# Kernel optimization log

Hardware: AMD Instinct MI355X
Metric: run time of the kernel (lower is better)

## Reference

```python
import jax, jax.numpy as jnp
import numpy as np

SCALING = 32.0 / 16  # alpha / rank


def setup_inputs() -> dict:
    key = jax.random.key(0)
    k1, k2, k3, k4, k5 = jax.random.split(key, 5)
    B, S, D_IN, D_OUT, R = 4, 2048, 4096, 4096, 16
    inputs = jax.random.normal(k1, (B, S, D_IN), dtype=jnp.float32)
    weight = jax.random.normal(k2, (D_OUT, D_IN), dtype=jnp.float32) * (1.0 / np.sqrt(D_IN))
    bias = jax.random.normal(k3, (D_OUT,), dtype=jnp.float32)
    lora_a = jax.random.normal(k4, (R, D_IN), dtype=jnp.float32) * (1.0 / np.sqrt(D_IN))
    lora_b = jax.random.normal(k5, (D_OUT, R), dtype=jnp.float32) * (1.0 / np.sqrt(R))
    return {"inputs": inputs, "weight": weight, "bias": bias, "lora_a": lora_a, "lora_b": lora_b}


def reference(inputs, weight, bias, lora_a, lora_b):
    # base = x @ W^T + b
    base = jnp.einsum("bsd,od->bso", inputs, weight) + bias
    # low-rank update: x @ (B A)^T * s, computed as two skinny matmuls
    # (mathematically identical to torch's full-rank materialization)
    xa = jnp.einsum("bsd,rd->bsr", inputs, lora_a)   # [B,S,R]
    update = jnp.einsum("bsr,or->bso", xa, lora_b)    # [B,S,O]
    return base + update * SCALING
```

## Files before the change

### kernel.cpp

```cpp
#include <hip/hip_runtime.h>
#include <hip/hip_bf16.h>
#include <stdint.h>


typedef __bf16 bf16x8 __attribute__((ext_vector_type(8)));
typedef __bf16 bf16x4 __attribute__((ext_vector_type(4)));
typedef float f32x4 __attribute__((ext_vector_type(4)));

#define LORA_R 16

__device__ __forceinline__ void async_copy16(const void* g, void* l) {
  __builtin_amdgcn_global_load_lds(
      (const __attribute__((address_space(1))) void*)g,
      (__attribute__((address_space(3))) void*)l, 16, 0, 0);
}


__global__ __launch_bounds__(256) void pack_x_kernel(
    const float* __restrict__ X, __hip_bfloat16* __restrict__ Xp, int K) {
  const int lane = threadIdx.x & 63;
  const int wave = threadIdx.x >> 6;
  const int nkb = K >> 5;
  const int kb = blockIdx.x * 4 + wave;
  const int mb = blockIdx.y;
  const int row = (mb << 4) + (lane & 15);
  const int col = (kb << 5) + ((lane >> 4) << 3);
  const float* src = X + (size_t)row * K + col;
  f32x4 v0 = *(const f32x4*)src;
  f32x4 v1 = *(const f32x4*)(src + 4);
  bf16x8 o;
#pragma unroll
  for (int j = 0; j < 4; ++j) { o[j] = (__bf16)v0[j]; o[4 + j] = (__bf16)v1[j]; }
  *(bf16x8*)((char*)Xp + ((size_t)(mb * nkb + kb) << 10) + (lane << 4)) = o;
}

__global__ __launch_bounds__(256) void foldpack_w_kernel(
    const float* __restrict__ W, const float* __restrict__ A,
    const float* __restrict__ Bl, __hip_bfloat16* __restrict__ Wp, int K) {
  const int lane = threadIdx.x & 63;
  const int wave = threadIdx.x >> 6;
  const int nkb = K >> 5;
  const int kb = blockIdx.x * 4 + wave;
  const int nb = blockIdx.y;
  const int n = (nb << 4) + (lane & 15);
  const int col = (kb << 5) + ((lane >> 4) << 3);
  float res[8];
  {
    f32x4 w0 = *(const f32x4*)(W + (size_t)n * K + col);
    f32x4 w1 = *(const f32x4*)(W + (size_t)n * K + col + 4);
#pragma unroll
    for (int j = 0; j < 4; ++j) { res[j] = w0[j]; res[4 + j] = w1[j]; }
  }
#pragma unroll
  for (int r = 0; r < LORA_R; ++r) {
    const float b2 = 2.0f * Bl[n * LORA_R + r];
    f32x4 a0 = *(const f32x4*)(A + (size_t)r * K + col);
    f32x4 a1 = *(const f32x4*)(A + (size_t)r * K + col + 4);
#pragma unroll
    for (int j = 0; j < 4; ++j) { res[j] += b2 * a0[j]; res[4 + j] += b2 * a1[j]; }
  }
  bf16x8 o;
#pragma unroll
  for (int j = 0; j < 8; ++j) o[j] = (__bf16)res[j];
  *(bf16x8*)((char*)Wp + ((size_t)(nb * nkb + kb) << 10) + (lane << 4)) = o;
}

__global__ __launch_bounds__(512, 2) void gemm_pipelined(
    const __hip_bfloat16* __restrict__ Xp,
    const __hip_bfloat16* __restrict__ Wp,
    const float* __restrict__ bias,
    float* __restrict__ Out, int M, int N, int K) {
  __shared__ __align__(16) char lds[131072];

  const int tid = threadIdx.x;
  const int lane = tid & 63;
  const int wave = tid >> 6;
  const int wm = wave >> 2;
  const int wn = wave & 3;

  const int nwg = gridDim.x;
  const int bid = blockIdx.x;
  const int swz = (bid & 7) * (nwg >> 3) + (bid >> 3);
  const int ntn = N >> 8;
  const int tm = swz / ntn;
  const int tn = swz - tm * ntn;

  const int nkb = K >> 5;
  const int nt = nkb;

  const char* aSrc = (const char*)Xp +
      ((size_t)((tm << 4) + wave) * nkb << 10) + (lane << 4);
  const char* bSrc = (const char*)Wp +
      ((size_t)((tn << 4) + wave) * nkb << 10) + (lane << 4);
  const size_t siteStride = (size_t)8 * nkb << 10;

  char* ldsA = lds + (wave << 10);
  char* ldsB = lds + 16384 + (wave << 10);
  const char* ldsRdA = lds + (wm << 13) + (lane << 4);
  const char* ldsRdB = lds + 16384 + (wn << 12) + (lane << 4);

  f32x4 acc[8][4];
#pragma unroll
  for (int i = 0; i < 8; ++i)
#pragma unroll
    for (int j = 0; j < 4; ++j) acc[i][j] = (f32x4){0.f, 0.f, 0.f, 0.f};

#pragma unroll
  for (int pt = 0; pt < 3; ++pt) {
    const int bo = pt << 15;
    async_copy16(aSrc + ((size_t)pt << 10), ldsA + bo);
    async_copy16(aSrc + siteStride + ((size_t)pt << 10), ldsA + bo + 8192);
    async_copy16(bSrc + ((size_t)pt << 10), ldsB + bo);
    async_copy16(bSrc + siteStride + ((size_t)pt << 10), ldsB + bo + 8192);
  }
  asm volatile("s_waitcnt vmcnt(8)" ::: "memory");
  __builtin_amdgcn_s_barrier();

  bf16x8 af[4], bv[4];
  for (int t = 0; t < nt - 3; ++t) {
    const int buf = t & 3;
    const int pb = (t + 3) & 3;
    const size_t kOff = (size_t)(t + 3) << 10;
    const char* aP = ldsRdA + (buf << 15);
    const char* bP = ldsRdB + (buf << 15);
#pragma unroll
    for (int i = 0; i < 4; ++i) af[i] = *(const bf16x8*)(aP + (i << 10));
#pragma unroll
    for (int i = 0; i < 4; ++i) bv[i] = *(const bf16x8*)(bP + (i << 10));
    async_copy16(aSrc + kOff, ldsA + (pb << 15));
    async_copy16(aSrc + siteStride + kOff, ldsA + (pb << 15) + 8192);
    __builtin_amdgcn_s_barrier();
    asm volatile("s_waitcnt lgkmcnt(0)" ::: "memory");
    __builtin_amdgcn_sched_barrier(0);
    __builtin_amdgcn_s_setprio(1);
#pragma unroll
    for (int mi = 0; mi < 4; ++mi)
#pragma unroll
      for (int ni = 0; ni < 4; ++ni)
        acc[mi][ni] = __builtin_amdgcn_mfma_f32_16x16x32_bf16(
            af[mi], bv[ni], acc[mi][ni], 0, 0, 0);
    __builtin_amdgcn_s_setprio(0);
    __builtin_amdgcn_s_barrier();
#pragma unroll
    for (int i = 0; i < 4; ++i) af[i] = *(const bf16x8*)(aP + 4096 + (i << 10));
    async_copy16(bSrc + kOff, ldsB + (pb << 15));
    async_copy16(bSrc + siteStride + kOff, ldsB + (pb << 15) + 8192);
    asm volatile("s_waitcnt vmcnt(8)" ::: "memory");
    __builtin_amdgcn_s_barrier();
    asm volatile("s_waitcnt lgkmcnt(0)" ::: "memory");
    __builtin_amdgcn_sched_barrier(0);
    __builtin_amdgcn_s_setprio(1);
#pragma unroll
    for (int mi = 0; mi < 4; ++mi)
#pragma unroll
      for (int ni = 0; ni < 4; ++ni)
        acc[4 + mi][ni] = __builtin_amdgcn_mfma_f32_16x16x32_bf16(
            af[mi], bv[ni], acc[4 + mi][ni], 0, 0, 0);
    __builtin_amdgcn_s_setprio(0);
    __builtin_amdgcn_s_barrier();
  }
  asm volatile("s_waitcnt vmcnt(0)" ::: "memory");
  __builtin_amdgcn_s_barrier();
  for (int t = nt - 3; t < nt; ++t) {
    const int buf = t & 3;
    const char* aP = ldsRdA + (buf << 15);
    const char* bP = ldsRdB + (buf << 15);
#pragma unroll
    for (int i = 0; i < 4; ++i) af[i] = *(const bf16x8*)(aP + (i << 10));
#pragma unroll
    for (int i = 0; i < 4; ++i) bv[i] = *(const bf16x8*)(bP + (i << 10));
#pragma unroll
    for (int mi = 0; mi < 4; ++mi)
#pragma unroll
      for (int ni = 0; ni < 4; ++ni)
        acc[mi][ni] = __builtin_amdgcn_mfma_f32_16x16x32_bf16(
            af[mi], bv[ni], acc[mi][ni], 0, 0, 0);
#pragma unroll
    for (int i = 0; i < 4; ++i) af[i] = *(const bf16x8*)(aP + 4096 + (i << 10));
#pragma unroll
    for (int mi = 0; mi < 4; ++mi)
#pragma unroll
      for (int ni = 0; ni < 4; ++ni)
        acc[4 + mi][ni] = __builtin_amdgcn_mfma_f32_16x16x32_bf16(
            af[mi], bv[ni], acc[4 + mi][ni], 0, 0, 0);
  }

  const int col = lane & 15;
  const int quad = lane >> 4;
  const int m0 = tm << 8;
  const int n0 = tn << 8;
#pragma unroll
  for (int ni = 0; ni < 4; ++ni) {
    const int n = n0 + wn * 64 + ni * 16 + col;
    const float bvs = bias[n];
#pragma unroll
    for (int mi = 0; mi < 8; ++mi) {
      const size_t rowBase = (size_t)(m0 + wm * 128 + mi * 16 + quad * 4) * N + n;
#pragma unroll
      for (int r = 0; r < 4; ++r)
        Out[rowBase + (size_t)r * N] = acc[mi][ni][r] + bvs;
    }
  }
}

#define BM 128
#define BN 128
#define BK 32

__global__ void foldcast_w_kernel(const float* __restrict__ W,
                                  const float* __restrict__ A,
                                  const float* __restrict__ Bl,
                                  __hip_bfloat16* __restrict__ Wp, int K) {
  const int n = blockIdx.y;
  const int k = blockIdx.x * 256 + threadIdx.x;
  float acc = W[(size_t)n * K + k];
#pragma unroll
  for (int r = 0; r < LORA_R; ++r)
    acc += 2.0f * Bl[n * LORA_R + r] * A[(size_t)r * K + k];
  Wp[(size_t)n * K + k] = __float2bfloat16(acc);
}

__global__ void padb32_kernel(const float* __restrict__ lB,
                              __hip_bfloat16* __restrict__ B32) {
  const int i = blockIdx.x * 256 + threadIdx.x;
  const int n = i >> 5, r = i & 31;
  B32[i] = (r < LORA_R) ? __float2bfloat16(lB[n * LORA_R + r])
                        : __float2bfloat16(0.0f);
}

__global__ __launch_bounds__(256) void xa_fp32_kernel(
    const float* __restrict__ X, const float* __restrict__ A,
    __hip_bfloat16* __restrict__ XA32, int K) {
  const int lane = threadIdx.x & 63;
  const int m = blockIdx.x * 4 + (threadIdx.x >> 6);
  float acc[LORA_R] = {};
  const size_t xrow = (size_t)m * K;
  for (int k0 = 0; k0 < K; k0 += 256) {
    const int k = k0 + lane * 4;
    f32x4 xv = *(const f32x4*)(X + xrow + k);
#pragma unroll
    for (int r = 0; r < LORA_R; ++r) {
      f32x4 av = *(const f32x4*)(A + (size_t)r * K + k);
      acc[r] += xv[0] * av[0] + xv[1] * av[1] + xv[2] * av[2] + xv[3] * av[3];
    }
  }
#pragma unroll
  for (int r = 0; r < LORA_R; ++r)
    for (int off = 32; off > 0; off >>= 1) acc[r] += __shfl_xor(acc[r], off, 64);
  if (lane == 0) {
#pragma unroll
    for (int r = 0; r < LORA_R; ++r)
      XA32[(size_t)m * 32 + r] = __float2bfloat16(acc[r]);
#pragma unroll
    for (int r = LORA_R; r < 32; ++r)
      XA32[(size_t)m * 32 + r] = __float2bfloat16(0.0f);
  }
}

template <bool XPRE, bool WPRE, bool ELORA>
__global__ __launch_bounds__(256) void gemm_kernel(
    const void* __restrict__ Xv, const void* __restrict__ Wv,
    const float* __restrict__ bias,
    const __hip_bfloat16* __restrict__ XA32,
    const __hip_bfloat16* __restrict__ B32,
    float* __restrict__ Out, int M, int N, int K) {
  __shared__ __align__(16) unsigned short As[BM * BK];
  __shared__ __align__(16) unsigned short Bs[BN * BK];

  const int t = threadIdx.x;
  const int lane = t & 63;
  const int wave = t >> 6;
  const int m0 = blockIdx.y * BM;
  const int n0 = blockIdx.x * BN;
  const int wm = (wave >> 1) * 64;
  const int wn = (wave & 1) * 64;

  const int srow = t >> 2;
  const int ka = (t & 3) * 8;
  const int f_r = t >> 3;
  const int f_c = (t & 7) * 4;

  char* smA = (char*)As;
  char* smB = (char*)Bs;
  const int waveByte = wave * 1024;

  f32x4 acc[4][4];
#pragma unroll
  for (int mi = 0; mi < 4; ++mi)
#pragma unroll
    for (int ni = 0; ni < 4; ++ni) acc[mi][ni] = (f32x4){0.f, 0.f, 0.f, 0.f};

  const unsigned short* aBase = As + (wm + (lane & 15)) * BK + (lane >> 4) * 8;
  const unsigned short* bBase = Bs + (wn + (lane & 15)) * BK + (lane >> 4) * 8;

  const int kIters = K / BK;
  for (int kt = 0; kt < kIters; ++kt) {
    const int gk = kt * BK;
    if constexpr (XPRE) {
      const __hip_bfloat16* Xb = (const __hip_bfloat16*)Xv;
      async_copy16(Xb + (size_t)(m0 + srow) * K + gk + ka, smA + waveByte);
      async_copy16(Xb + (size_t)(m0 + 64 + srow) * K + gk + ka, smA + 4096 + waveByte);
    } else {
      const float* Xf = (const float*)Xv;
#pragma unroll
      for (int j = 0; j < 4; ++j) {
        const int row = j * 32 + f_r;
        f32x4 v = *(const f32x4*)(Xf + (size_t)(m0 + row) * K + gk + f_c);
        bf16x4 p;
#pragma unroll
        for (int e = 0; e < 4; ++e) p[e] = (__bf16)v[e];
        *(bf16x4*)(smA + row * 64 + f_c * 2) = p;
      }
    }
    if constexpr (WPRE) {
      const __hip_bfloat16* Wb = (const __hip_bfloat16*)Wv;
      async_copy16(Wb + (size_t)(n0 + srow) * K + gk + ka, smB + waveByte);
      async_copy16(Wb + (size_t)(n0 + 64 + srow) * K + gk + ka, smB + 4096 + waveByte);
    } else {
      const float* Wf = (const float*)Wv;
#pragma unroll
      for (int j = 0; j < 4; ++j) {
        const int row = j * 32 + f_r;
        f32x4 v = *(const f32x4*)(Wf + (size_t)(n0 + row) * K + gk + f_c);
        bf16x4 p;
#pragma unroll
        for (int e = 0; e < 4; ++e) p[e] = (__bf16)v[e];
        *(bf16x4*)(smB + row * 64 + f_c * 2) = p;
      }
    }
    __syncthreads();

    bf16x8 af[4], bfv[4];
#pragma unroll
    for (int i = 0; i < 4; ++i) {
      af[i] = *(const bf16x8*)(aBase + i * 16 * BK);
      bfv[i] = *(const bf16x8*)(bBase + i * 16 * BK);
    }
#pragma unroll
    for (int mi = 0; mi < 4; ++mi)
#pragma unroll
      for (int ni = 0; ni < 4; ++ni)
        acc[mi][ni] = __builtin_amdgcn_mfma_f32_16x16x32_bf16(
            af[mi], bfv[ni], acc[mi][ni], 0, 0, 0);
    __syncthreads();
  }

  const int col = lane & 15;
  const int quad = lane >> 4;
  const int rbase = quad * 4;

  bf16x8 xaf[4], blf[4];
  if constexpr (ELORA) {
#pragma unroll
    for (int mi = 0; mi < 4; ++mi)
      xaf[mi] = *(const bf16x8*)(XA32 + (size_t)(m0 + wm + mi * 16 + col) * 32 + quad * 8);
#pragma unroll
    for (int ni = 0; ni < 4; ++ni)
      blf[ni] = *(const bf16x8*)(B32 + (size_t)(n0 + wn + ni * 16 + col) * 32 + quad * 8);
  }

  const f32x4 zero4 = (f32x4){0.f, 0.f, 0.f, 0.f};
#pragma unroll
  for (int ni = 0; ni < 4; ++ni) {
    const int n = n0 + wn + ni * 16 + col;
    const float bv = bias[n];
#pragma unroll
    for (int mi = 0; mi < 4; ++mi) {
      f32x4 u = zero4;
      if constexpr (ELORA)
        u = __builtin_amdgcn_mfma_f32_16x16x32_bf16(xaf[mi], blf[ni], zero4, 0, 0, 0);
      const size_t rowBase = (size_t)(m0 + wm + mi * 16 + rbase) * N + n;
#pragma unroll
      for (int r = 0; r < 4; ++r)
        Out[rowBase + (size_t)r * N] = acc[mi][ni][r] + bv + 2.0f * u[r];
    }
  }
}

extern "C" void kernel_launch(void* const* d_in, const int* in_sizes, int n_in,
                              void* d_out, int out_size, void* d_ws, size_t ws_size,
                              hipStream_t stream) {
  const float* X    = (const float*)d_in[0];
  const float* W    = (const float*)d_in[1];
  const float* bias = (const float*)d_in[2];
  const float* lA   = (const float*)d_in[3];
  const float* lB   = (const float*)d_in[4];
  float* Out = (float*)d_out;

  const int K = in_sizes[3] / LORA_R;
  const int N = in_sizes[2];
  const int M = in_sizes[0] / K;

  const size_t xbBytes = (size_t)M * K * 2;
  const size_t wpBytes = (size_t)N * K * 2;

  if (ws_size >= xbBytes + wpBytes) {
    __hip_bfloat16* Xp = (__hip_bfloat16*)d_ws;
    __hip_bfloat16* Wq = (__hip_bfloat16*)((char*)d_ws + xbBytes);
    pack_x_kernel<<<dim3(K / 128, M / 16), 256, 0, stream>>>(X, Xp, K);
    foldpack_w_kernel<<<dim3(K / 128, N / 16), 256, 0, stream>>>(W, lA, lB, Wq, K);
    gemm_pipelined<<<dim3((M / 256) * (N / 256)), 512, 0, stream>>>(
        Xp, Wq, bias, Out, M, N, K);
  } else if (ws_size >= wpBytes) {
    __hip_bfloat16* Wp = (__hip_bfloat16*)d_ws;
    foldcast_w_kernel<<<dim3(K / 256, N), 256, 0, stream>>>(W, lA, lB, Wp, K);
    gemm_kernel<false, true, false><<<dim3(N / BN, M / BM), 256, 0, stream>>>(
        X, Wp, bias, nullptr, nullptr, Out, M, N, K);
  } else {
    __hip_bfloat16* XA32 = (__hip_bfloat16*)d_ws;
    __hip_bfloat16* B32  = XA32 + (size_t)M * 32;
    padb32_kernel<<<dim3((N * 32) / 256), 256, 0, stream>>>(lB, B32);
    xa_fp32_kernel<<<dim3(M / 4), 256, 0, stream>>>(X, lA, XA32, K);
    gemm_kernel<false, false, true><<<dim3(N / BN, M / BM), 256, 0, stream>>>(
        X, W, bias, XA32, B32, Out, M, N, K);
  }
}
```

Baseline: 525.3 us.

## Double-buffer LDS fragment reads in registers to overlap with MFMA in GEMM loop

Restructures the main GEMM loop into a two-step unrolled schedule. The A/B fragments for the next half-tile are read from LDS into a second register set while MFMAs run on the current set. Full lgkmcnt(0) waits become partial waits, and the global-to-LDS staging is interleaved so LDS latency overlaps matrix-core work. The tail is rewritten to stage the last tile and then drain the remaining four tiles. This adds register pressure and more intricate waitcnt/barrier ordering, which risks spills or subtle hazards.

New measurement: 519.7 us. Within noise of the previous version (-1.1%).

```diff
diff --git a/kernel.cpp b/kernel.cpp
--- a/kernel.cpp
+++ b/kernel.cpp
@@ -14,7 +14,6 @@
       (const __attribute__((address_space(1))) void*)g,
       (__attribute__((address_space(3))) void*)l, 16, 0, 0);
 }
-
 
 __global__ __launch_bounds__(256) void pack_x_kernel(
     const float* __restrict__ X, __hip_bfloat16* __restrict__ Xp, int K) {
@@ -65,6 +64,46 @@
   *(bf16x8*)((char*)Wp + ((size_t)(nb * nkb + kb) << 10) + (lane << 4)) = o;
 }
 
+#define RD_A4(v0, v1, v2, v3, OFF)                                            \
+  v0 = *(const bf16x8*)(ldsRdA + (OFF));                                      \
+  v1 = *(const bf16x8*)(ldsRdA + (OFF) + 1024);                               \
+  v2 = *(const bf16x8*)(ldsRdA + (OFF) + 2048);                               \
+  v3 = *(const bf16x8*)(ldsRdA + (OFF) + 3072);
+
+#define RD_B4(v0, v1, v2, v3, OFF)                                            \
+  v0 = *(const bf16x8*)(ldsRdB + (OFF));                                      \
+  v1 = *(const bf16x8*)(ldsRdB + (OFF) + 1024);                               \
+  v2 = *(const bf16x8*)(ldsRdB + (OFF) + 2048);                               \
+  v3 = *(const bf16x8*)(ldsRdB + (OFF) + 3072);
+
+#define MFMA16(BASE, A0, A1, A2, A3, B0, B1, B2, B3)                          \
+  acc[BASE + 0][0] = __builtin_amdgcn_mfma_f32_16x16x32_bf16(A0, B0, acc[BASE + 0][0], 0, 0, 0); \
+  acc[BASE + 0][1] = __builtin_amdgcn_mfma_f32_16x16x32_bf16(A0, B1, acc[BASE + 0][1], 0, 0, 0); \
+  acc[BASE + 0][2] = __builtin_amdgcn_mfma_f32_16x16x32_bf16(A0, B2, acc[BASE + 0][2], 0, 0, 0); \
+  acc[BASE + 0][3] = __builtin_amdgcn_mfma_f32_16x16x32_bf16(A0, B3, acc[BASE + 0][3], 0, 0, 0); \
+  acc[BASE + 1][0] = __builtin_amdgcn_mfma_f32_16x16x32_bf16(A1, B0, acc[BASE + 1][0], 0, 0, 0); \
+  acc[BASE + 1][1] = __builtin_amdgcn_mfma_f32_16x16x32_bf16(A1, B1, acc[BASE + 1][1], 0, 0, 0); \
+  acc[BASE + 1][2] = __builtin_amdgcn_mfma_f32_16x16x32_bf16(A1, B2, acc[BASE + 1][2], 0, 0, 0); \
+  acc[BASE + 1][3] = __builtin_amdgcn_mfma_f32_16x16x32_bf16(A1, B3, acc[BASE + 1][3], 0, 0, 0); \
+  acc[BASE + 2][0] = __builtin_amdgcn_mfma_f32_16x16x32_bf16(A2, B0, acc[BASE + 2][0], 0, 0, 0); \
+  acc[BASE + 2][1] = __builtin_amdgcn_mfma_f32_16x16x32_bf16(A2, B1, acc[BASE + 2][1], 0, 0, 0); \
+  acc[BASE + 2][2] = __builtin_amdgcn_mfma_f32_16x16x32_bf16(A2, B2, acc[BASE + 2][2], 0, 0, 0); \
+  acc[BASE + 2][3] = __builtin_amdgcn_mfma_f32_16x16x32_bf16(A2, B3, acc[BASE + 2][3], 0, 0, 0); \
+  acc[BASE + 3][0] = __builtin_amdgcn_mfma_f32_16x16x32_bf16(A3, B0, acc[BASE + 3][0], 0, 0, 0); \
+  acc[BASE + 3][1] = __builtin_amdgcn_mfma_f32_16x16x32_bf16(A3, B1, acc[BASE + 3][1], 0, 0, 0); \
+  acc[BASE + 3][2] = __builtin_amdgcn_mfma_f32_16x16x32_bf16(A3, B2, acc[BASE + 3][2], 0, 0, 0); \
+  acc[BASE + 3][3] = __builtin_amdgcn_mfma_f32_16x16x32_bf16(A3, B3, acc[BASE + 3][3], 0, 0, 0);
+
+#define STAGE_A(T3, SLOT)                                                     \
+  async_copy16(aSrc + ((size_t)(T3) << 10), ldsA + (SLOT));                   \
+  async_copy16(aSrc + siteStride + ((size_t)(T3) << 10), ldsA + (SLOT) + 8192);
+
+#define STAGE_B(T3, SLOT)                                                     \
+  async_copy16(bSrc + ((size_t)(T3) << 10), ldsB + (SLOT));                   \
+  async_copy16(bSrc + siteStride + ((size_t)(T3) << 10), ldsB + (SLOT) + 8192);
+
+#define SBAR() __builtin_amdgcn_sched_barrier(0)
+
 __global__ __launch_bounds__(512, 2) void gemm_pipelined(
     const __hip_bfloat16* __restrict__ Xp,
     const __hip_bfloat16* __restrict__ Wp,
@@ -115,74 +154,90 @@
   }
   asm volatile("s_waitcnt vmcnt(8)" ::: "memory");
   __builtin_amdgcn_s_barrier();
-
-  bf16x8 af[4], bv[4];
-  for (int t = 0; t < nt - 3; ++t) {
-    const int buf = t & 3;
-    const int pb = (t + 3) & 3;
-    const size_t kOff = (size_t)(t + 3) << 10;
-    const char* aP = ldsRdA + (buf << 15);
-    const char* bP = ldsRdB + (buf << 15);
-#pragma unroll
-    for (int i = 0; i < 4; ++i) af[i] = *(const bf16x8*)(aP + (i << 10));
-#pragma unroll
-    for (int i = 0; i < 4; ++i) bv[i] = *(const bf16x8*)(bP + (i << 10));
-    async_copy16(aSrc + kOff, ldsA + (pb << 15));
-    async_copy16(aSrc + siteStride + kOff, ldsA + (pb << 15) + 8192);
+  SBAR();
+
+  bf16x8 aE0, aE1, aE2, aE3, aO0, aO1, aO2, aO3, a10, a11, a12, a13;
+  bf16x8 bE0, bE1, bE2, bE3, bO0, bO1, bO2, bO3;
+
+  RD_A4(aE0, aE1, aE2, aE3, 0);
+  RD_B4(bE0, bE1, bE2, bE3, 0);
+
+  for (int e = 0; e + 5 <= nt; e += 2) {
+    const int ofsE = (e & 3) << 15;
+    const int ofsO = ((e + 1) & 3) << 15;
+    const int ofsN = ((e + 2) & 3) << 15;
+    const int s3 = ((e + 3) & 3) << 15;
+    const int s4 = ((e + 4) & 3) << 15;
+
+    RD_A4(a10, a11, a12, a13, ofsE + 4096);
+    STAGE_A(e + 3, s3);
+    asm volatile("s_waitcnt lgkmcnt(4)" ::: "memory");
+    SBAR();
+    __builtin_amdgcn_s_setprio(1);
+    MFMA16(0, aE0, aE1, aE2, aE3, bE0, bE1, bE2, bE3);
+    __builtin_amdgcn_s_setprio(0);
+    asm volatile("s_waitcnt vmcnt(6)" ::: "memory");
     __builtin_amdgcn_s_barrier();
-    asm volatile("s_waitcnt lgkmcnt(0)" ::: "memory");
-    __builtin_amdgcn_sched_barrier(0);
+    SBAR();
+
+    RD_A4(aO0, aO1, aO2, aO3, ofsO);
+    RD_B4(bO0, bO1, bO2, bO3, ofsO);
+    STAGE_B(e + 3, s3);
+    asm volatile("s_waitcnt lgkmcnt(8)" ::: "memory");
+    SBAR();
     __builtin_amdgcn_s_setprio(1);
-#pragma unroll
-    for (int mi = 0; mi < 4; ++mi)
-#pragma unroll
-      for (int ni = 0; ni < 4; ++ni)
-        acc[mi][ni] = __builtin_amdgcn_mfma_f32_16x16x32_bf16(
-            af[mi], bv[ni], acc[mi][ni], 0, 0, 0);
+    MFMA16(4, a10, a11, a12, a13, bE0, bE1, bE2, bE3);
     __builtin_amdgcn_s_setprio(0);
     __builtin_amdgcn_s_barrier();
-#pragma unroll
-    for (int i = 0; i < 4; ++i) af[i] = *(const bf16x8*)(aP + 4096 + (i << 10));
-    async_copy16(bSrc + kOff, ldsB + (pb << 15));
-    async_copy16(bSrc + siteStride + kOff, ldsB + (pb << 15) + 8192);
-    asm volatile("s_waitcnt vmcnt(8)" ::: "memory");
+    SBAR();
+
+    RD_A4(a10, a11, a12, a13, ofsO + 4096);
+    STAGE_A(e + 4, s4);
+    asm volatile("s_waitcnt lgkmcnt(4)" ::: "memory");
+    SBAR();
+    __builtin_amdgcn_s_setprio(1);
+    MFMA16(0, aO0, aO1, aO2, aO3, bO0, bO1, bO2, bO3);
+    __builtin_amdgcn_s_setprio(0);
+    asm volatile("s_waitcnt vmcnt(6)" ::: "memory");
     __builtin_amdgcn_s_barrier();
-    asm volatile("s_waitcnt lgkmcnt(0)" ::: "memory");
-    __builtin_amdgcn_sched_barrier(0);
+    SBAR();
+
+    RD_A4(aE0, aE1, aE2, aE3, ofsN);
+    RD_B4(bE0, bE1, bE2, bE3, ofsN);
+    STAGE_B(e + 4, s4);
+    asm volatile("s_waitcnt lgkmcnt(8)" ::: "memory");
+    SBAR();
     __builtin_amdgcn_s_setprio(1);
-#pragma unroll
-    for (int mi = 0; mi < 4; ++mi)
-#pragma unroll
-      for (int ni = 0; ni < 4; ++ni)
-        acc[4 + mi][ni] = __builtin_amdgcn_mfma_f32_16x16x32_bf16(
-            af[mi], bv[ni], acc[4 + mi][ni], 0, 0, 0);
+    MFMA16(4, a10, a11, a12, a13, bO0, bO1, bO2, bO3);
     __builtin_amdgcn_s_setprio(0);
     __builtin_amdgcn_s_barrier();
-  }
-  asm volatile("s_waitcnt vmcnt(0)" ::: "memory");
-  __builtin_amdgcn_s_barrier();
-  for (int t = nt - 3; t < nt; ++t) {
-    const int buf = t & 3;
-    const char* aP = ldsRdA + (buf << 15);
-    const char* bP = ldsRdB + (buf << 15);
-#pragma unroll
-    for (int i = 0; i < 4; ++i) af[i] = *(const bf16x8*)(aP + (i << 10));
-#pragma unroll
-    for (int i = 0; i < 4; ++i) bv[i] = *(const bf16x8*)(bP + (i << 10));
-#pragma unroll
-    for (int mi = 0; mi < 4; ++mi)
-#pragma unroll
-      for (int ni = 0; ni < 4; ++ni)
-        acc[mi][ni] = __builtin_amdgcn_mfma_f32_16x16x32_bf16(
-            af[mi], bv[ni], acc[mi][ni], 0, 0, 0);
-#pragma unroll
-    for (int i = 0; i < 4; ++i) af[i] = *(const bf16x8*)(aP + 4096 + (i << 10));
-#pragma unroll
-    for (int mi = 0; mi < 4; ++mi)
-#pragma unroll
-      for (int ni = 0; ni < 4; ++ni)
-        acc[4 + mi][ni] = __builtin_amdgcn_mfma_f32_16x16x32_bf16(
-            af[mi], bv[ni], acc[4 + mi][ni], 0, 0, 0);
+    SBAR();
+  }
+
+  {
+    const int tL = nt - 1;
+    const int sL = (tL & 3) << 15;
+    STAGE_A(tL, sL);
+    STAGE_B(tL, sL);
+    asm volatile("s_waitcnt vmcnt(0)" ::: "memory");
+    __builtin_amdgcn_s_barrier();
+    SBAR();
+    for (int t = nt - 4; t < nt; ++t) {
+      const int ofs = (t & 3) << 15;
+      bf16x8 af[8], bv4[4];
+#pragma unroll
+      for (int i = 0; i < 8; ++i)
+        af[i] = *(const bf16x8*)(ldsRdA + ofs + (i << 10));
+#pragma unroll
+      for (int i = 0; i < 4; ++i)
+        bv4[i] = *(const bf16x8*)(ldsRdB + ofs + (i << 10));
+#pragma unroll
+      for (int mi = 0; mi < 8; ++mi)
+#pragma unroll
+        for (int ni = 0; ni < 4; ++ni)
+          acc[mi][ni] = __builtin_amdgcn_mfma_f32_16x16x32_bf16(
+              af[mi], bv4[ni], acc[mi][ni], 0, 0, 0);
+    }
   }
 
   const int col = lane & 15;
```

## Switch GEMM to 32x32x16 MFMA with matching packed layout and register double-buffering

Applied to the files above, without the earlier changes.

Replaces the 16x16x32 bf16 MFMA tiles with 32x32x16 MFMA, and repacks X and W into a 32-row by 16-k fragment layout using a cross-lane shuffle in the pack kernels. The main loop now double-buffers fragment registers so the LDS reads for the next half-step overlap the current MFMA batch, with finer lgkmcnt and vmcnt waits. Larger MFMA tiles cut LDS fragment traffic and instruction count per FLOP. The epilogue is rewritten for the 32x32 accumulator layout, and the tighter wait counts add correctness risk.

After: 539.6 us. +2.7%, slower.

```diff
diff --git a/kernel.cpp b/kernel.cpp
--- a/kernel.cpp
+++ b/kernel.cpp
@@ -6,6 +6,8 @@
 typedef __bf16 bf16x8 __attribute__((ext_vector_type(8)));
 typedef __bf16 bf16x4 __attribute__((ext_vector_type(4)));
 typedef float f32x4 __attribute__((ext_vector_type(4)));
+typedef float f32x16 __attribute__((ext_vector_type(16)));
+typedef int i32x4 __attribute__((ext_vector_type(4)));
 
 #define LORA_R 16
 
@@ -20,18 +22,23 @@
     const float* __restrict__ X, __hip_bfloat16* __restrict__ Xp, int K) {
   const int lane = threadIdx.x & 63;
   const int wave = threadIdx.x >> 6;
-  const int nkb = K >> 5;
-  const int kb = blockIdx.x * 4 + wave;
-  const int mb = blockIdx.y;
-  const int row = (mb << 4) + (lane & 15);
-  const int col = (kb << 5) + ((lane >> 4) << 3);
-  const float* src = X + (size_t)row * K + col;
+  const int nkblk = K >> 4;
+  const int kblk = blockIdx.x * 4 + wave;
+  const int rb = blockIdx.y;
+  const int srow = rb * 32 + (lane >> 1);
+  const int scol = kblk * 16 + (lane & 1) * 8;
+  const float* src = X + (size_t)srow * K + scol;
   f32x4 v0 = *(const f32x4*)src;
   f32x4 v1 = *(const f32x4*)(src + 4);
   bf16x8 o;
 #pragma unroll
   for (int j = 0; j < 4; ++j) { o[j] = (__bf16)v0[j]; o[4 + j] = (__bf16)v1[j]; }
-  *(bf16x8*)((char*)Xp + ((size_t)(mb * nkb + kb) << 10) + (lane << 4)) = o;
+  const int s = ((lane & 31) << 1) | (lane >> 5);
+  i32x4 wv = __builtin_bit_cast(i32x4, o);
+  i32x4 rv;
+#pragma unroll
+  for (int d = 0; d < 4; ++d) rv[d] = __shfl(wv[d], s, 64);
+  *(i32x4*)((char*)Xp + ((size_t)(rb * nkblk + kblk) << 10) + (lane << 4)) = rv;
 }
 
 __global__ __launch_bounds__(256) void foldpack_w_kernel(
@@ -39,11 +46,11 @@
     const float* __restrict__ Bl, __hip_bfloat16* __restrict__ Wp, int K) {
   const int lane = threadIdx.x & 63;
   const int wave = threadIdx.x >> 6;
-  const int nkb = K >> 5;
-  const int kb = blockIdx.x * 4 + wave;
+  const int nkblk = K >> 4;
+  const int kblk = blockIdx.x * 4 + wave;
   const int nb = blockIdx.y;
-  const int n = (nb << 4) + (lane & 15);
-  const int col = (kb << 5) + ((lane >> 4) << 3);
+  const int n = nb * 32 + (lane >> 1);
+  const int col = kblk * 16 + (lane & 1) * 8;
   float res[8];
   {
     f32x4 w0 = *(const f32x4*)(W + (size_t)n * K + col);
@@ -62,8 +69,41 @@
   bf16x8 o;
 #pragma unroll
   for (int j = 0; j < 8; ++j) o[j] = (__bf16)res[j];
-  *(bf16x8*)((char*)Wp + ((size_t)(nb * nkb + kb) << 10) + (lane << 4)) = o;
-}
+  const int s = ((lane & 31) << 1) | (lane >> 5);
+  i32x4 wv = __builtin_bit_cast(i32x4, o);
+  i32x4 rv;
+#pragma unroll
+  for (int d = 0; d < 4; ++d) rv[d] = __shfl(wv[d], s, 64);
+  *(i32x4*)((char*)Wp + ((size_t)(nb * nkblk + kblk) << 10) + (lane << 4)) = rv;
+}
+
+#define RD6(AV, BV, KB, OFS)                                                  \
+  AV[0] = *(const bf16x8*)(ldsRdA + (OFS) + (KB) * 1024 + 0 * 2048);          \
+  AV[1] = *(const bf16x8*)(ldsRdA + (OFS) + (KB) * 1024 + 1 * 2048);          \
+  AV[2] = *(const bf16x8*)(ldsRdA + (OFS) + (KB) * 1024 + 2 * 2048);          \
+  AV[3] = *(const bf16x8*)(ldsRdA + (OFS) + (KB) * 1024 + 3 * 2048);          \
+  BV[0] = *(const bf16x8*)(ldsRdB + (OFS) + (KB) * 1024 + 0 * 2048);          \
+  BV[1] = *(const bf16x8*)(ldsRdB + (OFS) + (KB) * 1024 + 1 * 2048);
+
+#define MFMA8(AV, BV)                                                         \
+  acc[0][0] = __builtin_amdgcn_mfma_f32_32x32x16_bf16(AV[0], BV[0], acc[0][0], 0, 0, 0); \
+  acc[0][1] = __builtin_amdgcn_mfma_f32_32x32x16_bf16(AV[0], BV[1], acc[0][1], 0, 0, 0); \
+  acc[1][0] = __builtin_amdgcn_mfma_f32_32x32x16_bf16(AV[1], BV[0], acc[1][0], 0, 0, 0); \
+  acc[1][1] = __builtin_amdgcn_mfma_f32_32x32x16_bf16(AV[1], BV[1], acc[1][1], 0, 0, 0); \
+  acc[2][0] = __builtin_amdgcn_mfma_f32_32x32x16_bf16(AV[2], BV[0], acc[2][0], 0, 0, 0); \
+  acc[2][1] = __builtin_amdgcn_mfma_f32_32x32x16_bf16(AV[2], BV[1], acc[2][1], 0, 0, 0); \
+  acc[3][0] = __builtin_amdgcn_mfma_f32_32x32x16_bf16(AV[3], BV[0], acc[3][0], 0, 0, 0); \
+  acc[3][1] = __builtin_amdgcn_mfma_f32_32x32x16_bf16(AV[3], BV[1], acc[3][1], 0, 0, 0);
+
+#define STAGE_A(T, SLOT)                                                      \
+  async_copy16(aSrc + ((size_t)(T) << 11), ldsA + (SLOT));                    \
+  async_copy16(aSrc + ((size_t)(T) << 11) + 1024, ldsA + (SLOT) + 1024);
+
+#define STAGE_B(T, SLOT)                                                      \
+  async_copy16(bSrc + ((size_t)(T) << 11), ldsB + (SLOT));                    \
+  async_copy16(bSrc + ((size_t)(T) << 11) + 1024, ldsB + (SLOT) + 1024);
+
+#define SBAR() __builtin_amdgcn_sched_barrier(0)
 
 __global__ __launch_bounds__(512, 2) void gemm_pipelined(
     const __hip_bfloat16* __restrict__ Xp,
@@ -85,120 +125,107 @@
   const int tm = swz / ntn;
   const int tn = swz - tm * ntn;
 
-  const int nkb = K >> 5;
-  const int nt = nkb;
+  const int nkblk = K >> 4;
+  const int nt = K >> 5;
 
   const char* aSrc = (const char*)Xp +
-      ((size_t)((tm << 4) + wave) * nkb << 10) + (lane << 4);
+      ((size_t)((tm << 3) + wave) * nkblk << 10) + (lane << 4);
   const char* bSrc = (const char*)Wp +
-      ((size_t)((tn << 4) + wave) * nkb << 10) + (lane << 4);
-  const size_t siteStride = (size_t)8 * nkb << 10;
-
-  char* ldsA = lds + (wave << 10);
-  char* ldsB = lds + 16384 + (wave << 10);
+      ((size_t)((tn << 3) + wave) * nkblk << 10) + (lane << 4);
+
+  char* ldsA = lds + (wave << 11);
+  char* ldsB = lds + 16384 + (wave << 11);
   const char* ldsRdA = lds + (wm << 13) + (lane << 4);
   const char* ldsRdB = lds + 16384 + (wn << 12) + (lane << 4);
 
-  f32x4 acc[8][4];
-#pragma unroll
-  for (int i = 0; i < 8; ++i)
-#pragma unroll
-    for (int j = 0; j < 4; ++j) acc[i][j] = (f32x4){0.f, 0.f, 0.f, 0.f};
+  f32x16 acc[4][2];
+#pragma unroll
+  for (int i = 0; i < 4; ++i)
+#pragma unroll
+    for (int j = 0; j < 2; ++j) acc[i][j] = (f32x16)(0.f);
 
 #pragma unroll
   for (int pt = 0; pt < 3; ++pt) {
     const int bo = pt << 15;
-    async_copy16(aSrc + ((size_t)pt << 10), ldsA + bo);
-    async_copy16(aSrc + siteStride + ((size_t)pt << 10), ldsA + bo + 8192);
-    async_copy16(bSrc + ((size_t)pt << 10), ldsB + bo);
-    async_copy16(bSrc + siteStride + ((size_t)pt << 10), ldsB + bo + 8192);
+    STAGE_A(pt, bo);
+    STAGE_B(pt, bo);
   }
   asm volatile("s_waitcnt vmcnt(8)" ::: "memory");
   __builtin_amdgcn_s_barrier();
-
-  bf16x8 af[4], bv[4];
-  for (int t = 0; t < nt - 3; ++t) {
-    const int buf = t & 3;
-    const int pb = (t + 3) & 3;
-    const size_t kOff = (size_t)(t + 3) << 10;
-    const char* aP = ldsRdA + (buf << 15);
-    const char* bP = ldsRdB + (buf << 15);
-#pragma unroll
-    for (int i = 0; i < 4; ++i) af[i] = *(const bf16x8*)(aP + (i << 10));
-#pragma unroll
-    for (int i = 0; i < 4; ++i) bv[i] = *(const bf16x8*)(bP + (i << 10));
-    async_copy16(aSrc + kOff, ldsA + (pb << 15));
-    async_copy16(aSrc + siteStride + kOff, ldsA + (pb << 15) + 8192);
+  SBAR();
+
+  bf16x8 aP[4], bP[2], aQ[4], bQ[2];
+  RD6(aP, bP, 0, 0);
+
+  for (int t = 0; t + 4 <= nt; ++t) {
+    const int ofs = (t & 3) << 15;
+    const int ofsN = ((t + 1) & 3) << 15;
+    const int s3 = ((t + 3) & 3) << 15;
+
+    RD6(aQ, bQ, 1, ofs);
+    STAGE_A(t + 3, s3);
+    asm volatile("s_waitcnt lgkmcnt(6)" ::: "memory");
+    SBAR();
+    __builtin_amdgcn_s_setprio(1);
+    MFMA8(aP, bP);
+    __builtin_amdgcn_s_setprio(0);
+    asm volatile("s_waitcnt vmcnt(6)" ::: "memory");
     __builtin_amdgcn_s_barrier();
-    asm volatile("s_waitcnt lgkmcnt(0)" ::: "memory");
-    __builtin_amdgcn_sched_barrier(0);
+    SBAR();
+
+    RD6(aP, bP, 0, ofsN);
+    STAGE_B(t + 3, s3);
+    asm volatile("s_waitcnt lgkmcnt(6)" ::: "memory");
+    SBAR();
     __builtin_amdgcn_s_setprio(1);
-#pragma unroll
-    for (int mi = 0; mi < 4; ++mi)
-#pragma unroll
-      for (int ni = 0; ni < 4; ++ni)
-        acc[mi][ni] = __builtin_amdgcn_mfma_f32_16x16x32_bf16(
-            af[mi], bv[ni], acc[mi][ni], 0, 0, 0);
+    MFMA8(aQ, bQ);
     __builtin_amdgcn_s_setprio(0);
     __builtin_amdgcn_s_barrier();
-#pragma unroll
-    for (int i = 0; i < 4; ++i) af[i] = *(const bf16x8*)(aP + 4096 + (i << 10));
-    async_copy16(bSrc + kOff, ldsB + (pb << 15));
-    async_copy16(bSrc + siteStride + kOff, ldsB + (pb << 15) + 8192);
-    asm volatile("s_waitcnt vmcnt(8)" ::: "memory");
-    __builtin_amdgcn_s_barrier();
-    asm volatile("s_waitcnt lgkmcnt(0)" ::: "memory");
-    __builtin_amdgcn_sched_barrier(0);
-    __builtin_amdgcn_s_setprio(1);
-#pragma unroll
-    for (int mi = 0; mi < 4; ++mi)
-#pragma unroll
-      for (int ni = 0; ni < 4; ++ni)
-        acc[4 + mi][ni] = __builtin_amdgcn_mfma_f32_16x16x32_bf16(
-            af[mi], bv[ni], acc[4 + mi][ni], 0, 0, 0);
-    __builtin_amdgcn_s_setprio(0);
-    __builtin_amdgcn_s_barrier();
-  }
+    SBAR();
+  }
+
   asm volatile("s_waitcnt vmcnt(0)" ::: "memory");
   __builtin_amdgcn_s_barrier();
+  SBAR();
   for (int t = nt - 3; t < nt; ++t) {
-    const int buf = t & 3;
-    const char* aP = ldsRdA + (buf << 15);
-    const char* bP = ldsRdB + (buf << 15);
-#pragma unroll
-    for (int i = 0; i < 4; ++i) af[i] = *(const bf16x8*)(aP + (i << 10));
-#pragma unroll
-    for (int i = 0; i < 4; ++i) bv[i] = *(const bf16x8*)(bP + (i << 10));
-#pragma unroll
-    for (int mi = 0; mi < 4; ++mi)
-#pragma unroll
-      for (int ni = 0; ni < 4; ++ni)
-        acc[mi][ni] = __builtin_amdgcn_mfma_f32_16x16x32_bf16(
-            af[mi], bv[ni], acc[mi][ni], 0, 0, 0);
-#pragma unroll
-    for (int i = 0; i < 4; ++i) af[i] = *(const bf16x8*)(aP + 4096 + (i << 10));
-#pragma unroll
-    for (int mi = 0; mi < 4; ++mi)
-#pragma unroll
-      for (int ni = 0; ni < 4; ++ni)
-        acc[4 + mi][ni] = __builtin_amdgcn_mfma_f32_16x16x32_bf16(
-            af[mi], bv[ni], acc[4 + mi][ni], 0, 0, 0);
-  }
-
-  const int col = lane & 15;
-  const int quad = lane >> 4;
+    const int ofs = (t & 3) << 15;
+    bf16x8 aT[4][2], bT[2][2];
+#pragma unroll
+    for (int i = 0; i < 4; ++i)
+#pragma unroll
+      for (int kb = 0; kb < 2; ++kb)
+        aT[i][kb] = *(const bf16x8*)(ldsRdA + ofs + (i * 2 + kb) * 1024);
+#pragma unroll
+    for (int j = 0; j < 2; ++j)
+#pragma unroll
+      for (int kb = 0; kb < 2; ++kb)
+        bT[j][kb] = *(const bf16x8*)(ldsRdB + ofs + (j * 2 + kb) * 1024);
+#pragma unroll
+    for (int kb = 0; kb < 2; ++kb)
+#pragma unroll
+      for (int i = 0; i < 4; ++i)
+#pragma unroll
+        for (int j = 0; j < 2; ++j)
+          acc[i][j] = __builtin_amdgcn_mfma_f32_32x32x16_bf16(
+              aT[i][kb], bT[j][kb], acc[i][j], 0, 0, 0);
+  }
+
+  const int colL = lane & 31;
+  const int hi = lane >> 5;
   const int m0 = tm << 8;
   const int n0 = tn << 8;
 #pragma unroll
-  for (int ni = 0; ni < 4; ++ni) {
-    const int n = n0 + wn * 64 + ni * 16 + col;
+  for (int j = 0; j < 2; ++j) {
+    const int n = n0 + wn * 64 + j * 32 + colL;
     const float bvs = bias[n];
 #pragma unroll
-    for (int mi = 0; mi < 8; ++mi) {
-      const size_t rowBase = (size_t)(m0 + wm * 128 + mi * 16 + quad * 4) * N + n;
-#pragma unroll
-      for (int r = 0; r < 4; ++r)
-        Out[rowBase + (size_t)r * N] = acc[mi][ni][r] + bvs;
+    for (int i = 0; i < 4; ++i) {
+      const int rowb = m0 + wm * 128 + i * 32 + hi * 4;
+#pragma unroll
+      for (int q = 0; q < 4; ++q)
+#pragma unroll
+        for (int r = 0; r < 4; ++r)
+          Out[(size_t)(rowb + q * 8 + r) * N + n] = acc[i][j][q * 4 + r] + bvs;
     }
   }
 }
@@ -397,8 +424,8 @@
   if (ws_size >= xbBytes + wpBytes) {
     __hip_bfloat16* Xp = (__hip_bfloat16*)d_ws;
     __hip_bfloat16* Wq = (__hip_bfloat16*)((char*)d_ws + xbBytes);
-    pack_x_kernel<<<dim3(K / 128, M / 16), 256, 0, stream>>>(X, Xp, K);
-    foldpack_w_kernel<<<dim3(K / 128, N / 16), 256, 0, stream>>>(W, lA, lB, Wq, K);
+    pack_x_kernel<<<dim3(K / 64, M / 32), 256, 0, stream>>>(X, Xp, K);
+    foldpack_w_kernel<<<dim3(K / 64, N / 32), 256, 0, stream>>>(W, lA, lB, Wq, K);
     gemm_pipelined<<<dim3((M / 256) * (N / 256)), 512, 0, stream>>>(
         Xp, Wq, bias, Out, M, N, K);
   } else if (ws_size >= wpBytes) {
```

## Double-buffer MFMA fragments in registers and cut barriers per k-step

Applied to the files above, without the earlier changes.

Restructures the GEMM main loop so each k-step reads the next tile's A and B fragments from LDS into a second register set while the MFMAs run on the current set. The two half-steps, each with two workgroup barriers, become one full 8x4 MFMA block with a single barrier. Both A and B async copies are issued together, and the vmcnt and lgkmcnt waits are retuned to match. This aims to hide LDS read latency and reduce synchronisation stalls. The cost is higher VGPR pressure from the extra fragment registers, which may hurt occupancy at launch bounds of 512 threads with 2 blocks.

New measurement: 520.4 us. No clear change (-0.9%).

```diff
diff --git a/kernel.cpp b/kernel.cpp
--- a/kernel.cpp
+++ b/kernel.cpp
@@ -14,7 +14,6 @@
       (const __attribute__((address_space(1))) void*)g,
       (__attribute__((address_space(3))) void*)l, 16, 0, 0);
 }
-
 
 __global__ __launch_bounds__(256) void pack_x_kernel(
     const float* __restrict__ X, __hip_bfloat16* __restrict__ Xp, int K) {
@@ -65,6 +64,43 @@
   *(bf16x8*)((char*)Wp + ((size_t)(nb * nkb + kb) << 10) + (lane << 4)) = o;
 }
 
+#define STAGE_A(T, SLOT)                                                      \
+  async_copy16(aSrc + ((size_t)(T) << 10), ldsA + (SLOT));                    \
+  async_copy16(aSrc + siteStride + ((size_t)(T) << 10), ldsA + (SLOT) + 8192);
+
+#define STAGE_B(T, SLOT)                                                      \
+  async_copy16(bSrc + ((size_t)(T) << 10), ldsB + (SLOT));                    \
+  async_copy16(bSrc + siteStride + ((size_t)(T) << 10), ldsB + (SLOT) + 8192);
+
+#define SBAR() __builtin_amdgcn_sched_barrier(0)
+
+#define BODY(AC, BC, AN, BN, T)                                               \
+  {                                                                           \
+    const int _ofsN = (((T) + 1) & 3) << 15;                                  \
+    const int _s3 = (((T) + 3) & 3) << 15;                                    \
+    _Pragma("unroll")                                                         \
+    for (int _i = 0; _i < 8; ++_i)                                            \
+      AN[_i] = *(const bf16x8*)(ldsRdA + _ofsN + (_i << 10));                 \
+    _Pragma("unroll")                                                         \
+    for (int _j = 0; _j < 4; ++_j)                                            \
+      BN[_j] = *(const bf16x8*)(ldsRdB + _ofsN + (_j << 10));                 \
+    STAGE_A((T) + 3, _s3);                                                    \
+    STAGE_B((T) + 3, _s3);                                                    \
+    asm volatile("s_waitcnt lgkmcnt(12)" ::: "memory");                       \
+    SBAR();                                                                   \
+    __builtin_amdgcn_s_setprio(1);                                            \
+    _Pragma("unroll")                                                         \
+    for (int _mi = 0; _mi < 8; ++_mi)                                         \
+      _Pragma("unroll")                                                       \
+      for (int _ni = 0; _ni < 4; ++_ni)                                       \
+        acc[_mi][_ni] = __builtin_amdgcn_mfma_f32_16x16x32_bf16(              \
+            AC[_mi], BC[_ni], acc[_mi][_ni], 0, 0, 0);                        \
+    __builtin_amdgcn_s_setprio(0);                                            \
+    asm volatile("s_waitcnt vmcnt(4)" ::: "memory");                          \
+    __builtin_amdgcn_s_barrier();                                             \
+    SBAR();                                                                   \
+  }
+
 __global__ __launch_bounds__(512, 2) void gemm_pipelined(
     const __hip_bfloat16* __restrict__ Xp,
     const __hip_bfloat16* __restrict__ Wp,
@@ -108,81 +144,48 @@
 #pragma unroll
   for (int pt = 0; pt < 3; ++pt) {
     const int bo = pt << 15;
-    async_copy16(aSrc + ((size_t)pt << 10), ldsA + bo);
-    async_copy16(aSrc + siteStride + ((size_t)pt << 10), ldsA + bo + 8192);
-    async_copy16(bSrc + ((size_t)pt << 10), ldsB + bo);
-    async_copy16(bSrc + siteStride + ((size_t)pt << 10), ldsB + bo + 8192);
-  }
-  asm volatile("s_waitcnt vmcnt(8)" ::: "memory");
+    STAGE_A(pt, bo);
+    STAGE_B(pt, bo);
+  }
+  asm volatile("s_waitcnt vmcnt(4)" ::: "memory");
   __builtin_amdgcn_s_barrier();
-
-  bf16x8 af[4], bv[4];
-  for (int t = 0; t < nt - 3; ++t) {
-    const int buf = t & 3;
-    const int pb = (t + 3) & 3;
-    const size_t kOff = (size_t)(t + 3) << 10;
-    const char* aP = ldsRdA + (buf << 15);
-    const char* bP = ldsRdB + (buf << 15);
-#pragma unroll
-    for (int i = 0; i < 4; ++i) af[i] = *(const bf16x8*)(aP + (i << 10));
-#pragma unroll
-    for (int i = 0; i < 4; ++i) bv[i] = *(const bf16x8*)(bP + (i << 10));
-    async_copy16(aSrc + kOff, ldsA + (pb << 15));
-    async_copy16(aSrc + siteStride + kOff, ldsA + (pb << 15) + 8192);
+  SBAR();
+
+  bf16x8 aE[8], bE[4], aO[8], bO[4];
+#pragma unroll
+  for (int i = 0; i < 8; ++i) aE[i] = *(const bf16x8*)(ldsRdA + (i << 10));
+#pragma unroll
+  for (int j = 0; j < 4; ++j) bE[j] = *(const bf16x8*)(ldsRdB + (j << 10));
+
+  for (int t = 0; t + 5 <= nt; t += 2) {
+    BODY(aE, bE, aO, bO, t);
+    BODY(aO, bO, aE, bE, t + 1);
+  }
+
+  {
+    const int tL = nt - 1;
+    const int sL = (tL & 3) << 15;
+    STAGE_A(tL, sL);
+    STAGE_B(tL, sL);
+    asm volatile("s_waitcnt vmcnt(0)" ::: "memory");
     __builtin_amdgcn_s_barrier();
-    asm volatile("s_waitcnt lgkmcnt(0)" ::: "memory");
-    __builtin_amdgcn_sched_barrier(0);
-    __builtin_amdgcn_s_setprio(1);
-#pragma unroll
-    for (int mi = 0; mi < 4; ++mi)
-#pragma unroll
-      for (int ni = 0; ni < 4; ++ni)
-        acc[mi][ni] = __builtin_amdgcn_mfma_f32_16x16x32_bf16(
-            af[mi], bv[ni], acc[mi][ni], 0, 0, 0);
-    __builtin_amdgcn_s_setprio(0);
-    __builtin_amdgcn_s_barrier();
-#pragma unroll
-    for (int i = 0; i < 4; ++i) af[i] = *(const bf16x8*)(aP + 4096 + (i << 10));
-    async_copy16(bSrc + kOff, ldsB + (pb << 15));
-    async_copy16(bSrc + siteStride + kOff, ldsB + (pb << 15) + 8192);
-    asm volatile("s_waitcnt vmcnt(8)" ::: "memory");
-    __builtin_amdgcn_s_barrier();
-    asm volatile("s_waitcnt lgkmcnt(0)" ::: "memory");
-    __builtin_amdgcn_sched_barrier(0);
-    __builtin_amdgcn_s_setprio(1);
-#pragma unroll
-    for (int mi = 0; mi < 4; ++mi)
-#pragma unroll
-      for (int ni = 0; ni < 4; ++ni)
-        acc[4 + mi][ni] = __builtin_amdgcn_mfma_f32_16x16x32_bf16(
-            af[mi], bv[ni], acc[4 + mi][ni], 0, 0, 0);
-    __builtin_amdgcn_s_setprio(0);
-    __builtin_amdgcn_s_barrier();
-  }
-  asm volatile("s_waitcnt vmcnt(0)" ::: "memory");
-  __builtin_amdgcn_s_barrier();
-  for (int t = nt - 3; t < nt; ++t) {
-    const int buf = t & 3;
-    const char* aP = ldsRdA + (buf << 15);
-    const char* bP = ldsRdB + (buf << 15);
-#pragma unroll
-    for (int i = 0; i < 4; ++i) af[i] = *(const bf16x8*)(aP + (i << 10));
-#pragma unroll
-    for (int i = 0; i < 4; ++i) bv[i] = *(const bf16x8*)(bP + (i << 10));
-#pragma unroll
-    for (int mi = 0; mi < 4; ++mi)
-#pragma unroll
-      for (int ni = 0; ni < 4; ++ni)
-        acc[mi][ni] = __builtin_amdgcn_mfma_f32_16x16x32_bf16(
-            af[mi], bv[ni], acc[mi][ni], 0, 0, 0);
-#pragma unroll
-    for (int i = 0; i < 4; ++i) af[i] = *(const bf16x8*)(aP + 4096 + (i << 10));
-#pragma unroll
-    for (int mi = 0; mi < 4; ++mi)
-#pragma unroll
-      for (int ni = 0; ni < 4; ++ni)
-        acc[4 + mi][ni] = __builtin_amdgcn_mfma_f32_16x16x32_bf16(
-            af[mi], bv[ni], acc[4 + mi][ni], 0, 0, 0);
+    SBAR();
+    for (int t = nt - 4; t < nt; ++t) {
+      const int ofs = (t & 3) << 15;
+      bf16x8 aT[8], bT[4];
+#pragma unroll
+      for (int i = 0; i < 8; ++i)
+        aT[i] = *(const bf16x8*)(ldsRdA + ofs + (i << 10));
+#pragma unroll
+      for (int j = 0; j < 4; ++j)
+        bT[j] = *(const bf16x8*)(ldsRdB + ofs + (j << 10));
+#pragma unroll
+      for (int mi = 0; mi < 8; ++mi)
+#pragma unroll
+        for (int ni = 0; ni < 4; ++ni)
+          acc[mi][ni] = __builtin_amdgcn_mfma_f32_16x16x32_bf16(
+              aT[mi], bT[ni], acc[mi][ni], 0, 0, 0);
+    }
   }
 
   const int col = lane & 15;
```
